# Kernel optimization log

Measured on AMD Instinct MI355X. Metric: run time of the kernel, lower is better.

The kernel has to match this reference:

```python
import jax, jax.numpy as jnp
import numpy as np

B, CIN, H, W = 8, 3, 128, 128
D_MODEL = 256
N_LAYERS = 4
D_STATE = 16
D_CONV = 4
EXPAND = 2
HEADDIM = 64
D_INNER = EXPAND * D_MODEL            # 512
NHEADS = D_INNER // HEADDIM           # 8
CONV_DIM = D_INNER + 2 * D_STATE      # 544
D_IN_PROJ = 2 * D_INNER + 2 * D_STATE + NHEADS  # 1064
D_OUT = 10
EPS = 1e-5


def setup_inputs() -> dict:
    key = jax.random.key(0)
    ks = iter(jax.random.split(key, 64))
    nrm = lambda shape, s=0.02: jax.random.normal(next(ks), shape, jnp.float32) * s
    L = N_LAYERS
    # dt init in [1e-3, 0.1], dt_bias = inverse softplus of dt
    dt = jnp.exp(jax.random.uniform(next(ks), (L, NHEADS)) * (np.log(0.1) - np.log(1e-3)) + np.log(1e-3))
    dt_bias = dt + jnp.log(-jnp.expm1(-dt))
    A_log = jnp.log(jax.random.uniform(next(ks), (L, NHEADS), minval=1.0, maxval=16.0))
    return {
        "x": jax.random.normal(next(ks), (B, CIN, H, W), jnp.float32),
        "stem_w1": nrm((D_MODEL // 2, CIN, 3, 3), 0.1),
        "stem_g1": jnp.ones((D_MODEL // 2,), jnp.float32),
        "stem_b1": jnp.zeros((D_MODEL // 2,), jnp.float32),
        "stem_w2": nrm((D_MODEL, D_MODEL // 2, 4, 4), 0.05),
        "stem_g2": jnp.ones((D_MODEL,), jnp.float32),
        "stem_b2": jnp.zeros((D_MODEL,), jnp.float32),
        "in_w": nrm((L, D_MODEL, D_IN_PROJ)),
        "conv_w": nrm((L, CONV_DIM, D_CONV), 0.2),
        "conv_b": jnp.zeros((L, CONV_DIM), jnp.float32),
        "dt_bias": dt_bias,
        "A_log": A_log,
        "D_skip": jnp.ones((L, NHEADS), jnp.float32),
        "rms_w": jnp.ones((L, D_INNER), jnp.float32),
        "out_w": nrm((L, D_INNER, D_MODEL)),
        "ln_g": jnp.ones((L, D_MODEL), jnp.float32),
        "ln_b": jnp.zeros((L, D_MODEL), jnp.float32),
        "head_ln_g": jnp.ones((D_MODEL,), jnp.float32),
        "head_ln_b": jnp.zeros((D_MODEL,), jnp.float32),
        "head_w": nrm((D_MODEL, D_OUT)),
        "head_b": jnp.zeros((D_OUT,), jnp.float32),
    }


def _bn(x, g, b):  # eval-mode BatchNorm2d with running mean 0 / var 1
    return x * g[None, :, None, None] + b[None, :, None, None]


def _ln(x, g, b):
    m = jnp.mean(x, -1, keepdims=True)
    v = jnp.mean((x - m) ** 2, -1, keepdims=True)
    return (x - m) * jax.lax.rsqrt(v + EPS) * g + b


def _mamba2(x, in_w, conv_w, conv_b, dt_bias, A_log, D_skip, rms_w, out_w):
    Bb, Lq, _ = x.shape
    zxbcdt = x @ in_w                                        # (B,L,D_IN_PROJ)
    z = zxbcdt[..., :D_INNER]
    xBC = zxbcdt[..., D_INNER:D_INNER + CONV_DIM]
    dt = jax.nn.softplus(zxbcdt[..., -NHEADS:] + dt_bias)    # (B,L,H)
    # causal depthwise conv1d over time
    xp = jnp.pad(xBC, ((0, 0), (D_CONV - 1, 0), (0, 0)))
    xBC = sum(xp[:, k:k + Lq, :] * conv_w[:, k] for k in range(D_CONV)) + conv_b
    xBC = jax.nn.silu(xBC)
    xs = xBC[..., :D_INNER].reshape(Bb, Lq, NHEADS, HEADDIM)       # (B,L,H,P)
    Bm = xBC[..., D_INNER:D_INNER + D_STATE]                        # (B,L,N)
    Cm = xBC[..., D_INNER + D_STATE:]                               # (B,L,N)
    dA = jnp.exp(dt * (-jnp.exp(A_log)))                            # (B,L,H)
    dtx = xs * dt[..., None]                                        # (B,L,H,P)

    def step(h, inp):  # h: (B,H,P,N)
        dA_t, dtx_t, B_t, C_t = inp
        h = h * dA_t[:, :, None, None] + dtx_t[..., None] * B_t[:, None, None, :]
        y = jnp.einsum('bhpn,bn->bhp', h, C_t)
        return h, y

    h0 = jnp.zeros((Bb, NHEADS, HEADDIM, D_STATE), x.dtype)
    seq = (jnp.moveaxis(dA, 1, 0), jnp.moveaxis(dtx, 1, 0),
           jnp.moveaxis(Bm, 1, 0), jnp.moveaxis(Cm, 1, 0))
    _, ys = jax.lax.scan(step, h0, seq)                             # (L,B,H,P)
    y = jnp.moveaxis(ys, 0, 1) + xs * D_skip[None, None, :, None]
    y = y.reshape(Bb, Lq, D_INNER)
    y = y * jax.nn.silu(z)                                          # gated
    y = y * jax.lax.rsqrt(jnp.mean(y * y, -1, keepdims=True) + EPS) * rms_w
    return y @ out_w


def reference(x, stem_w1, stem_g1, stem_b1, stem_w2, stem_g2, stem_b2,
              in_w, conv_w, conv_b, dt_bias, A_log, D_skip, rms_w, out_w,
              ln_g, ln_b, head_ln_g, head_ln_b, head_w, head_b):
    dn = ('NCHW', 'OIHW', 'NCHW')
    h = jax.lax.conv_general_dilated(x, stem_w1, (1, 1), 'SAME', dimension_numbers=dn)
    h = jax.nn.gelu(_bn(h, stem_g1, stem_b1), approximate=False)
    h = jax.lax.conv_general_dilated(h, stem_w2, (4, 4), 'VALID', dimension_numbers=dn)
    h = jax.nn.gelu(_bn(h, stem_g2, stem_b2), approximate=False)
    tok = h.reshape(h.shape[0], D_MODEL, -1).transpose(0, 2, 1)     # (B,L,D)
    for i in range(N_LAYERS):
        m = _mamba2(tok, in_w[i], conv_w[i], conv_b[i], dt_bias[i],
                    A_log[i], D_skip[i], rms_w[i], out_w[i])
        tok = _ln(m + tok, ln_g[i], ln_b[i])
    pooled = tok.mean(1)
    return _ln(pooled, head_ln_g, head_ln_b) @ head_w + head_b
```

## Files before the change

### kernel.cpp

```cpp
#include <hip/hip_runtime.h>
#include <hip/hip_bf16.h>


#define DEV __device__ __forceinline__
typedef __hip_bfloat16 bf16;
typedef unsigned short ushort_t;
typedef __attribute__((ext_vector_type(8))) short s8v;
typedef __attribute__((ext_vector_type(8))) unsigned short u8v;
typedef __attribute__((ext_vector_type(4))) unsigned short u4v;
typedef __attribute__((ext_vector_type(4))) float f4v;

#define CHUNK 32
#define NCH 32
#define YST 520

#define SP_CONVW 0
#define SP_CONVB 8704
#define SP_DTB   10880
#define SP_ALOG  10912
#define SP_DSK   10944
#define SP_RMSW  10976
#define SP_LNG   13024
#define SP_LNB   14048
#define SP_HLG   15072
#define SP_HLB   15328
#define SP_HW    15584
#define SP_HB    18144
#define SP_G1    18160
#define SP_B1    18288
#define SP_G2    18416
#define SP_B2    18672
#define SP_TOTAL 18928

DEV float bf2f(bf16 h) { return __bfloat162float(h); }
DEV bf16 f2bf(float f) { return __float2bfloat16(f); }
DEV float us2f(ushort_t u) { return __uint_as_float(((unsigned int)u) << 16); }
DEV ushort_t f2bfs(float f) {
    unsigned int u = __float_as_uint(f);
    return (ushort_t)((u + 0x7FFFu + ((u >> 16) & 1u)) >> 16);
}
DEV float ldf(const void* p, size_t i, int bf) {
    return bf ? us2f(((const ushort_t*)p)[i]) : ((const float*)p)[i];
}
DEV ushort_t ldbf(const void* p, size_t i, int bf) {
    return bf ? ((const ushort_t*)p)[i] : f2bfs(((const float*)p)[i]);
}
DEV int mode_of(const void* g1) { return (((const unsigned int*)g1)[0] == 0x3F800000u) ? 0 : 1; }
DEV float sigmoidf_(float x) { return 1.f / (1.f + __expf(-x)); }
DEV float geluf_(float x) { return 0.5f * x * (1.f + erff(x * 0.70710678118654752f)); }

__global__ void k_prep(const void* cw, const void* cb, const void* dtb, const void* alog,
                       const void* dsk, const void* rmsw, const void* lng, const void* lnb,
                       const void* hlg, const void* hlb, const void* hw, const void* hb,
                       const void* g1, const void* b1, const void* g2, const void* b2,
                       const void* w1, const void* w2, const void* inw, const void* outw,
                       float* __restrict__ sp, ushort_t* __restrict__ wT) {
    int md = mode_of(g1);
    int i = blockIdx.x * 256 + threadIdx.x;
    if (i < SP_TOTAL) {
        float v;
        if (i < SP_CONVB) v = ldf(cw, i, md);
        else if (i < SP_DTB) v = ldf(cb, i - SP_CONVB, md);
        else if (i < SP_ALOG) v = ldf(dtb, i - SP_DTB, md);
        else if (i < SP_DSK) v = ldf(alog, i - SP_ALOG, md);
        else if (i < SP_RMSW) v = ldf(dsk, i - SP_DSK, md);
        else if (i < SP_LNG) v = ldf(rmsw, i - SP_RMSW, md);
        else if (i < SP_LNB) v = ldf(lng, i - SP_LNG, md);
        else if (i < SP_HLG) v = ldf(lnb, i - SP_LNB, md);
        else if (i < SP_HLB) v = ldf(hlg, i - SP_HLG, md);
        else if (i < SP_HW) v = ldf(hlb, i - SP_HLB, md);
        else if (i < SP_HB) v = ldf(hw, i - SP_HW, md);
        else if (i < SP_G1) v = (i - SP_HB < 10) ? ldf(hb, i - SP_HB, md) : 0.f;
        else if (i < SP_B1) v = ldf(g1, i - SP_G1, md);
        else if (i < SP_G2) v = ldf(b1, i - SP_B1, md);
        else if (i < SP_B2) v = ldf(g2, i - SP_G2, md);
        else v = ldf(b2, i - SP_B2, md);
        sp[i] = v;
        return;
    }
    int iw = i - SP_TOTAL;
    if (iw >= 2142208) return;
    ushort_t v;
    if (iw < 4096) {
        int oc = iw >> 5, k = iw & 31;
        v = (k < 27) ? ldbf(w1, (size_t)oc * 27 + k, md) : 0;
    } else if (iw < 528384) {
        int j = iw - 4096;
        int oc = j >> 11, k = j & 2047;
        int c = k & 127, kykx = k >> 7;
        v = ldbf(w2, (size_t)(oc * 128 + c) * 16 + kykx, md);
    } else if (iw < 1617920) {
        int j = iw - 528384;
        int l = j / 272384, r = j % 272384;
        int n = r >> 8, k = r & 255;
        v = ldbf(inw, (size_t)l * 272384 + (size_t)k * 1064 + n, md);
    } else {
        int j = iw - 1617920;
        int l = j >> 17, r = j & 131071;
        int n = r >> 9, k = r & 511;
        v = ldbf(outw, (size_t)l * 131072 + (size_t)k * 256 + n, md);
    }
    wT[iw] = v;
}

template <int MD>
DEV void im2col_body(const void* x, ushort_t* __restrict__ Aim, int m) {
    int xx = m & 127;
    int y = (m >> 7) & 127;
    int b = m >> 14;
    ushort_t* o = Aim + (size_t)m * 32;
#pragma unroll
    for (int ci = 0; ci < 3; ci++)
#pragma unroll
        for (int dy = 0; dy < 3; dy++) {
            int sy = y + dy - 1;
#pragma unroll
            for (int dx = 0; dx < 3; dx++) {
                int sx = xx + dx - 1;
                ushort_t v = 0;
                if (sy >= 0 && sy < 128 && sx >= 0 && sx < 128) {
                    size_t idx = (size_t)((b * 3 + ci) * 128 + sy) * 128 + sx;
                    v = MD ? ((const ushort_t*)x)[idx] : f2bfs(((const float*)x)[idx]);
                }
                o[ci * 9 + dy * 3 + dx] = v;
            }
        }
#pragma unroll
    for (int k = 27; k < 32; k++) o[k] = 0;
}
__global__ void k_im2col(const void* __restrict__ x, ushort_t* __restrict__ Aim,
                         const void* __restrict__ g1) {
    int m = blockIdx.x * 256 + threadIdx.x;
    if (m >= 131072) return;
    if (mode_of(g1)) im2col_body<1>(x, Aim, m);
    else im2col_body<0>(x, Aim, m);
}

template <int EPI, int CBF, int BK>
__global__ __launch_bounds__(256, 3) void k_gemmT(const ushort_t* __restrict__ A,
                                                  const ushort_t* __restrict__ Wt, void* __restrict__ C,
                                                  int M, int N, int K, int klen,
                                                  const float* __restrict__ g, const float* __restrict__ bb) {
    constexpr int KG = BK / 8;
    constexpr int EA = BK / 4;
    constexpr int EB = BK / 2;
    constexpr int AU = EA / 8;
    constexpr int BU = EB / 8;
    __shared__ __align__(16) ushort_t As[2][64 * BK];
    __shared__ __align__(16) ushort_t Bs[2][128 * BK];
    int tid = threadIdx.x;
    int m0 = blockIdx.y * 64, n0 = blockIdx.x * 128;
    int koff = blockIdx.z * klen;
    int w = tid >> 6, lane = tid & 63;
    int wm = (w >> 1) * 32, wn = (w & 1) * 64;
    int lm = lane & 15, quad = lane >> 4;
    int ar = tid >> 2, ak = (tid & 3) * EA;
    int br = tid >> 1, bk = (tid & 1) * EB;
    bool bvalid = (n0 + br) < N;

    u8v pa[AU], pb[BU];
    auto loadT = [&](int kb) {
        const u8v* ap = (const u8v*)(A + (size_t)(m0 + ar) * K + koff + kb + ak);
#pragma unroll
        for (int j = 0; j < AU; j++) pa[j] = ap[j];
        if (bvalid) {
            const u8v* bp = (const u8v*)(Wt + (size_t)(n0 + br) * K + koff + kb + bk);
#pragma unroll
            for (int j = 0; j < BU; j++) pb[j] = bp[j];
        } else {
#pragma unroll
            for (int j = 0; j < BU; j++) pb[j] = (u8v)0;
        }
    };
    auto storeT = [&](int buf) {
        int ag = ak >> 3;
#pragma unroll
        for (int j = 0; j < AU; j++)
            *(u8v*)&As[buf][((ar >> 4) * KG + ag + j) * 128 + (ar & 15) * 8] = pa[j];
        int bg = bk >> 3;
#pragma unroll
        for (int j = 0; j < BU; j++)
            *(u8v*)&Bs[buf][((br >> 4) * KG + bg + j) * 128 + (br & 15) * 8] = pb[j];
    };

    f4v acc[2][4];
#pragma unroll
    for (int i = 0; i < 2; i++)
#pragma unroll
        for (int j = 0; j < 4; j++) acc[i][j] = (f4v){0.f, 0.f, 0.f, 0.f};

    int niter = klen / BK;
    loadT(0);
    storeT(0);
    if (niter > 1) loadT(BK);
    __syncthreads();
    for (int it = 0; it < niter; it++) {
        int buf = it & 1;
        if (it + 1 < niter) {
            storeT(buf ^ 1);
            if (it + 2 < niter) loadT((it + 2) * BK);
        }
#pragma unroll
        for (int kk = 0; kk < BK / 32; kk++) {
            s8v af[2], bfr[4];
#pragma unroll
            for (int i = 0; i < 2; i++)
                af[i] = *(const s8v*)&As[buf][(((wm >> 4) + i) * KG + kk * 4 + quad) * 128 + lm * 8];
#pragma unroll
            for (int j = 0; j < 4; j++)
                bfr[j] = *(const s8v*)&Bs[buf][(((wn >> 4) + j) * KG + kk * 4 + quad) * 128 + lm * 8];
#pragma unroll
            for (int i = 0; i < 2; i++)
#pragma unroll
                for (int j = 0; j < 4; j++)
                    acc[i][j] = __builtin_amdgcn_mfma_f32_16x16x32_bf16(af[i], bfr[j], acc[i][j], 0, 0, 0);
        }
        __syncthreads();
    }
    float* Cz = (float*)C + (size_t)blockIdx.z * M * N;
#pragma unroll
    for (int i = 0; i < 2; i++)
#pragma unroll
        for (int j = 0; j < 4; j++) {
            int nn = n0 + wn + j * 16 + lm;
            if (nn >= N) continue;
            float gv = (EPI >= 1) ? g[nn] : 0.f, bv = (EPI >= 1) ? bb[nn] : 0.f;
#pragma unroll
            for (int rr = 0; rr < 4; rr++) {
                int mm = m0 + wm + i * 16 + quad * 4 + rr;
                float v = acc[i][j][rr];
                if (EPI >= 1) v = geluf_(v * gv + bv);
                if (EPI == 2) {
                    int b = mm >> 14, y = (mm >> 7) & 127, x = mm & 127;
                    size_t mp = (size_t)(b * 1024 + (y >> 2) * 32 + (x >> 2));
                    ((bf16*)C)[mp * 2048 + ((y & 3) * 4 + (x & 3)) * 128 + nn] = f2bf(v);
                } else if (CBF) {
                    ((bf16*)C)[(size_t)mm * N + nn] = f2bf(v);
                } else {
                    Cz[(size_t)mm * N + nn] = v;
                }
            }
        }
}

__global__ __launch_bounds__(256) void k_stemred(const float* __restrict__ parts, const float* __restrict__ sp,
                                                 float* __restrict__ tok, ushort_t* __restrict__ tokb) {
    int m = blockIdx.x, c = threadIdx.x;
    size_t off = (size_t)m * 256 + c;
    float s = parts[off] + parts[2097152 + off];
    float v = geluf_(s * sp[SP_G2 + c] + sp[SP_B2 + c]);
    tok[off] = v;
    tokb[off] = f2bfs(v);
}

__global__ __launch_bounds__(64) void k_scan1(const bf16* __restrict__ zx, const float* __restrict__ sp,
                                              float* __restrict__ Sbuf, float* __restrict__ Pbuf, int layer) {
    int bid = blockIdx.x;
    int c = bid & (NCH - 1);
    int bh = bid >> 5;
    int b = bh >> 3, h = bh & 7;
    int p = threadIdx.x;
    __shared__ __align__(16) ushort_t zraw[35 * 64];
    __shared__ __align__(16) ushort_t braw[35 * 32];
    __shared__ float xs_s[CHUNK * 64];
    __shared__ __align__(16) float bc_s[CHUNK * 32];
    __shared__ float da_s[CHUNK], dt_s[CHUNK];
    const ushort_t* zxB = (const ushort_t*)zx + (size_t)b * 1024 * 1064;
    int t0 = c * CHUNK;
#pragma unroll
    for (int k = 0; k < 5; k++) {
        int j = p + k * 64;
        if (j < 280) {
            int row = j >> 3, c8 = j & 7;
            int t = t0 - 3 + row;
            u8v v = (u8v)0;
            if (t >= 0) v = *(const u8v*)(zxB + (size_t)t * 1064 + 512 + h * 64 + c8 * 8);
            *(u8v*)&zraw[row * 64 + c8 * 8] = v;
        }
    }
#pragma unroll
    for (int k = 0; k < 3; k++) {
        int j = p + k * 64;
        if (j < 140) {
            int row = j >> 2, c8 = j & 3;
            int t = t0 - 3 + row;
            u8v v = (u8v)0;
            if (t >= 0) v = *(const u8v*)(zxB + (size_t)t * 1064 + 1024 + c8 * 8);
            *(u8v*)&braw[row * 32 + c8 * 8] = v;
        }
    }
    if (p < CHUNK) {
        float raw = bf2f(zx[(size_t)(b * 1024 + t0 + p) * 1064 + 1056 + h]) + sp[SP_DTB + layer * 8 + h];
        float dt = raw > 20.f ? raw : log1pf(expf(raw));
        float a = expf(sp[SP_ALOG + layer * 8 + h]);
        dt_s[p] = dt;
        da_s[p] = expf(-dt * a);
    }
    __syncthreads();
    {
        const float* wp = sp + SP_CONVW + (size_t)(layer * 544 + h * 64 + p) * 4;
        float w0 = wp[0], w1 = wp[1], w2 = wp[2], w3 = wp[3];
        float bias = sp[SP_CONVB + layer * 544 + h * 64 + p];
#pragma unroll 8
        for (int tt = 0; tt < CHUNK; tt++) {
            float acc = bias + us2f(zraw[tt * 64 + p]) * w0 + us2f(zraw[(tt + 1) * 64 + p]) * w1 +
                        us2f(zraw[(tt + 2) * 64 + p]) * w2 + us2f(zraw[(tt + 3) * 64 + p]) * w3;
            xs_s[tt * 64 + p] = acc * sigmoidf_(acc);
        }
    }
    if (p < 32) {
        const float* wp = sp + SP_CONVW + (size_t)(layer * 544 + 512 + p) * 4;
        float w0 = wp[0], w1 = wp[1], w2 = wp[2], w3 = wp[3];
        float bias = sp[SP_CONVB + layer * 544 + 512 + p];
        int n = p & 15;
        int slot = (p < 16) ? 2 * n : 2 * n + 1;
#pragma unroll 8
        for (int tt = 0; tt < CHUNK; tt++) {
            float acc = bias + us2f(braw[tt * 32 + p]) * w0 + us2f(braw[(tt + 1) * 32 + p]) * w1 +
                        us2f(braw[(tt + 2) * 32 + p]) * w2 + us2f(braw[(tt + 3) * 32 + p]) * w3;
            bc_s[tt * 32 + slot] = acc * sigmoidf_(acc);
        }
    }
    __syncthreads();
    float hs[16];
#pragma unroll
    for (int n = 0; n < 16; n++) hs[n] = 0.f;
    float P = 1.f;
    for (int tt = 0; tt < CHUNK; tt++) {
        float xsv = xs_s[tt * 64 + p];
        float dAv = da_s[tt], dtv = dt_s[tt];
        P *= dAv;
        float dtx = xsv * dtv;
        const float4* bcp = (const float4*)&bc_s[tt * 32];
#pragma unroll
        for (int j = 0; j < 8; j++) {
            float4 v = bcp[j];
            hs[2 * j] = hs[2 * j] * dAv + dtx * v.x;
            hs[2 * j + 1] = hs[2 * j + 1] * dAv + dtx * v.z;
        }
    }
    float* So = Sbuf + (size_t)bid * 1024;
#pragma unroll
    for (int n = 0; n < 16; n++) So[n * 64 + p] = hs[n];
    if (p == 0) Pbuf[bid] = P;
}

__global__ __launch_bounds__(256) void k_scan2(const float* __restrict__ Sbuf, const float* __restrict__ Pbuf,
                                               float* __restrict__ Hbuf) {
    int bh = blockIdx.x >> 2;
    int e = ((blockIdx.x & 3) << 8) + threadIdx.x;
    const float* Sp = Sbuf + (size_t)bh * NCH * 1024 + e;
    float* Hp = Hbuf + (size_t)bh * NCH * 1024 + e;
    float hh = 0.f;
#pragma unroll
    for (int gq = 0; gq < 4; gq++) {
        float s[8];
#pragma unroll
        for (int c2 = 0; c2 < 8; c2++) s[c2] = Sp[(size_t)(gq * 8 + c2) * 1024];
#pragma unroll
        for (int c2 = 0; c2 < 8; c2++) {
            Hp[(size_t)(gq * 8 + c2) * 1024] = hh;
            float P = Pbuf[bh * NCH + gq * 8 + c2];
            hh = P * hh + s[c2];
        }
    }
}

__global__ __launch_bounds__(512, 2) void k_scan3go(const bf16* __restrict__ zx,
                                                    const float* __restrict__ Hbuf,
                                                    const float* __restrict__ sp,
                                                    const ushort_t* __restrict__ Wt,
                                                    float* __restrict__ tok, ushort_t* __restrict__ tokb,
                                                    int layer) {
    int bid = blockIdx.x;
    int c = bid & 31;
    int b = bid >> 5;
    int tid = threadIdx.x;
    int h = tid >> 6, p = tid & 63;
    __shared__ __align__(16) ushort_t zraw[35 * 512];
    __shared__ __align__(16) ushort_t braw[35 * 32];
    __shared__ __align__(16) float bc_s[CHUNK * 32];
    __shared__ float da_s[8 * CHUNK], dt_s[8 * CHUNK];
    const ushort_t* zxB = (const ushort_t*)zx + (size_t)b * 1024 * 1064;
    int t0 = c * CHUNK;

#pragma unroll
    for (int k = 0; k < 5; k++) {
        int j = tid + k * 512;
        if (j < 2240) {
            int row = j >> 6, c8 = j & 63;
            int t = t0 - 3 + row;
            u8v v = (u8v)0;
            if (t >= 0) v = *(const u8v*)(zxB + (size_t)t * 1064 + 512 + c8 * 8);
            *(u8v*)&zraw[row * 512 + c8 * 8] = v;
        }
    }
    if (tid < 140) {
        int row = tid >> 2, c8 = tid & 3;
        int t = t0 - 3 + row;
        u8v v = (u8v)0;
        if (t >= 0) v = *(const u8v*)(zxB + (size_t)t * 1064 + 1024 + c8 * 8);
        *(u8v*)&braw[row * 32 + c8 * 8] = v;
    }
    if (tid < 256) {
        int tt = tid >> 3, hh = tid & 7;
        float raw = bf2f(zx[(size_t)(b * 1024 + t0 + tt) * 1064 + 1056 + hh]) + sp[SP_DTB + layer * 8 + hh];
        float dtv = raw > 20.f ? raw : log1pf(expf(raw));
        float a = expf(sp[SP_ALOG + layer * 8 + hh]);
        dt_s[hh * 32 + tt] = dtv;
        da_s[hh * 32 + tt] = expf(-dtv * a);
    }
    __syncthreads();

    float xs[CHUNK];
    {
        float4 w4 = *(const float4*)(sp + SP_CONVW + (size_t)(layer * 544 + tid) * 4);
        float bias = sp[SP_CONVB + layer * 544 + tid];
#pragma unroll
        for (int tt = 0; tt < CHUNK; tt++) {
            float acc = bias + us2f(zraw[tt * 512 + tid]) * w4.x + us2f(zraw[(tt + 1) * 512 + tid]) * w4.y +
                        us2f(zraw[(tt + 2) * 512 + tid]) * w4.z + us2f(zraw[(tt + 3) * 512 + tid]) * w4.w;
            xs[tt] = acc * sigmoidf_(acc);
        }
    }
    if (tid < 32) {
        float4 w4 = *(const float4*)(sp + SP_CONVW + (size_t)(layer * 544 + 512 + tid) * 4);
        float bias = sp[SP_CONVB + layer * 544 + 512 + tid];
        int n = tid & 15;
        int slot = (tid < 16) ? 2 * n : 2 * n + 1;
#pragma unroll
        for (int tt = 0; tt < CHUNK; tt++) {
            float acc = bias + us2f(braw[tt * 32 + tid]) * w4.x + us2f(braw[(tt + 1) * 32 + tid]) * w4.y +
                        us2f(braw[(tt + 2) * 32 + tid]) * w4.z + us2f(braw[(tt + 3) * 32 + tid]) * w4.w;
            bc_s[tt * 32 + slot] = acc * sigmoidf_(acc);
        }
    }

    float hs[16];
    {
        const float* Si = Hbuf + ((size_t)(b * 8 + h) * 32 + c) * 1024;
#pragma unroll
        for (int n = 0; n < 16; n++) hs[n] = Si[n * 64 + p];
    }
    float dsk = sp[SP_DSK + layer * 8 + h];
    __syncthreads();

    ushort_t* y_s = zraw;
#pragma unroll
    for (int tt = 0; tt < CHUNK; tt++) {
        float dAv = da_s[h * 32 + tt], dtv = dt_s[h * 32 + tt];
        float dtx = xs[tt] * dtv;
        float acc = 0.f;
        const float4* bcp = (const float4*)&bc_s[tt * 32];
#pragma unroll
        for (int j = 0; j < 8; j++) {
            float4 v = bcp[j];
            hs[2 * j] = hs[2 * j] * dAv + dtx * v.x;
            acc += hs[2 * j] * v.y;
            hs[2 * j + 1] = hs[2 * j + 1] * dAv + dtx * v.z;
            acc += hs[2 * j + 1] * v.w;
        }
        y_s[tt * YST + tid] = f2bfs(acc + xs[tt] * dsk);
    }
    __syncthreads();

    {
        int lane = p;
        float4 rw0 = *(const float4*)(sp + SP_RMSW + layer * 512 + lane * 8);
        float4 rw1 = *(const float4*)(sp + SP_RMSW + layer * 512 + lane * 8 + 4);
        float rwv[8] = {rw0.x, rw0.y, rw0.z, rw0.w, rw1.x, rw1.y, rw1.z, rw1.w};
#pragma unroll
        for (int r = 0; r < 4; r++) {
            int tt = h * 4 + r;
            u8v yv = *(const u8v*)&y_s[tt * YST + lane * 8];
            u8v zv = *(const u8v*)(zxB + (size_t)(t0 + tt) * 1064 + lane * 8);
            float t[8];
            float ss = 0.f;
#pragma unroll
            for (int j2 = 0; j2 < 8; j2++) {
                float z = us2f(zv[j2]);
                float yy = us2f(yv[j2]);
                float tv = yy * (z * sigmoidf_(z));
                t[j2] = tv;
                ss += tv * tv;
            }
#pragma unroll
            for (int d = 32; d; d >>= 1) ss += __shfl_xor(ss, d, 64);
            float scale = rsqrtf(ss * (1.f / 512.f) + 1e-5f);
            u8v o;
#pragma unroll
            for (int j2 = 0; j2 < 8; j2++) o[j2] = f2bfs(t[j2] * scale * rwv[j2]);
            *(u8v*)&y_s[tt * YST + lane * 8] = o;
        }
    }
    __syncthreads();

    int lm = p & 15, quad = p >> 4;
    f4v acc2[2][2];
#pragma unroll
    for (int mi = 0; mi < 2; mi++)
#pragma unroll
        for (int ni = 0; ni < 2; ni++) acc2[mi][ni] = (f4v){0.f, 0.f, 0.f, 0.f};
#pragma unroll
    for (int kk = 0; kk < 16; kk++) {
        s8v af[2], bw[2];
#pragma unroll
        for (int mi = 0; mi < 2; mi++)
            af[mi] = *(const s8v*)&y_s[(mi * 16 + lm) * YST + kk * 32 + quad * 8];
#pragma unroll
        for (int ni = 0; ni < 2; ni++)
            bw[ni] = *(const s8v*)(Wt + (size_t)(h * 32 + ni * 16 + lm) * 512 + kk * 32 + quad * 8);
#pragma unroll
        for (int mi = 0; mi < 2; mi++)
#pragma unroll
            for (int ni = 0; ni < 2; ni++)
                acc2[mi][ni] = __builtin_amdgcn_mfma_f32_16x16x32_bf16(af[mi], bw[ni], acc2[mi][ni], 0, 0, 0);
    }
    __syncthreads();

    float* C_lds = (float*)zraw;
#pragma unroll
    for (int mi = 0; mi < 2; mi++)
#pragma unroll
        for (int ni = 0; ni < 2; ni++)
#pragma unroll
            for (int rr = 0; rr < 4; rr++)
                C_lds[(mi * 16 + quad * 4 + rr) * 260 + h * 32 + ni * 16 + lm] = acc2[mi][ni][rr];
    __syncthreads();

#pragma unroll
    for (int r = 0; r < 4; r++) {
        int tt = h * 4 + r;
        size_t off = (size_t)(b * 1024 + t0 + tt) * 256 + p * 4;
        float4 v = *(const float4*)(tok + off);
        float4 cv = *(const float4*)&C_lds[tt * 260 + p * 4];
        v.x += cv.x;
        v.y += cv.y;
        v.z += cv.z;
        v.w += cv.w;
        float s = v.x + v.y + v.z + v.w;
#pragma unroll
        for (int d = 32; d; d >>= 1) s += __shfl_xor(s, d, 64);
        float mean = s * (1.f / 256.f);
        float dx = v.x - mean, dy = v.y - mean, dz = v.z - mean, dw = v.w - mean;
        float ss = dx * dx + dy * dy + dz * dz + dw * dw;
#pragma unroll
        for (int d = 32; d; d >>= 1) ss += __shfl_xor(ss, d, 64);
        float inv = rsqrtf(ss * (1.f / 256.f) + 1e-5f);
        const float* lg = sp + SP_LNG + layer * 256 + p * 4;
        const float* lb = sp + SP_LNB + layer * 256 + p * 4;
        float r0 = dx * inv * lg[0] + lb[0];
        float r1 = dy * inv * lg[1] + lb[1];
        float r2 = dz * inv * lg[2] + lb[2];
        float r3 = dw * inv * lg[3] + lb[3];
        float4 rv;
        rv.x = r0; rv.y = r1; rv.z = r2; rv.w = r3;
        *(float4*)(tok + off) = rv;
        u4v ob;
        ob[0] = f2bfs(r0); ob[1] = f2bfs(r1); ob[2] = f2bfs(r2); ob[3] = f2bfs(r3);
        *(u4v*)(tokb + off) = ob;
    }
}

DEV float block_sum256(float v, float* s4) {
#pragma unroll
    for (int off = 32; off; off >>= 1) v += __shfl_down(v, off, 64);
    __syncthreads();
    if ((threadIdx.x & 63) == 0) s4[threadIdx.x >> 6] = v;
    __syncthreads();
    return s4[0] + s4[1] + s4[2] + s4[3];
}

__global__ void k_pool1(const float* __restrict__ tok, float* __restrict__ ppart) {
    int b = blockIdx.x >> 4, chunk = blockIdx.x & 15;
    int c = threadIdx.x;
    float s = 0.f;
    for (int t = 0; t < 64; t++) s += tok[((size_t)b * 1024 + chunk * 64 + t) * 256 + c];
    ppart[(size_t)blockIdx.x * 256 + c] = s;
}

__global__ __launch_bounds__(256) void k_head(const float* __restrict__ ppart, const float* __restrict__ sp,
                                              void* __restrict__ out, const void* __restrict__ g1) {
    __shared__ float s4[4];
    __shared__ float lds[256];
    int md = mode_of(g1);
    int b = blockIdx.x;
    int c = threadIdx.x;
    float v = 0.f;
#pragma unroll
    for (int k = 0; k < 16; k++) v += ppart[(size_t)(b * 16 + k) * 256 + c];
    v *= (1.f / 1024.f);
    float mean = block_sum256(v, s4) * (1.f / 256.f);
    float d = v - mean;
    float var = block_sum256(d * d, s4) * (1.f / 256.f);
    lds[c] = d * rsqrtf(var + 1e-5f) * sp[SP_HLG + c] + sp[SP_HLB + c];
    __syncthreads();
    if (c < 10) {
        float s = sp[SP_HB + c];
        for (int k = 0; k < 256; k++) s += lds[k] * sp[SP_HW + k * 10 + c];
        if (md)
            ((bf16*)out)[b * 10 + c] = f2bf(s);
        else
            ((float*)out)[b * 10 + c] = s;
    }
}

extern "C" void kernel_launch(void* const* d_in, const int* in_sizes, int n_in, void* d_out, int out_size,
                              void* d_ws, size_t ws_size, hipStream_t stream) {
    const void* x         = d_in[0];
    const void* stem_w1   = d_in[1];
    const void* stem_g1   = d_in[2];
    const void* stem_b1   = d_in[3];
    const void* stem_w2   = d_in[4];
    const void* stem_g2   = d_in[5];
    const void* stem_b2   = d_in[6];
    const void* in_w      = d_in[7];
    const void* conv_w    = d_in[8];
    const void* conv_b    = d_in[9];
    const void* dt_bias   = d_in[10];
    const void* A_log     = d_in[11];
    const void* D_skip    = d_in[12];
    const void* rms_w     = d_in[13];
    const void* out_w     = d_in[14];
    const void* ln_g      = d_in[15];
    const void* ln_b      = d_in[16];
    const void* head_ln_g = d_in[17];
    const void* head_ln_b = d_in[18];
    const void* head_w    = d_in[19];
    const void* head_b    = d_in[20];

    float* ws     = (float*)d_ws;
    float* tok    = ws;
    float* mbuf   = ws + 2097152;
    float* Hbuf   = ws + 4194304;
    float* parts  = ws + 6291456;
    float* ppart  = ws + 14682112;
    float* Pbuf   = ws + 14714880;
    float* sp     = ws + 14716944;
    ushort_t* tokb = (ushort_t*)(ws + 14735888);
    ushort_t* wT  = (ushort_t*)(ws + 15784464);
    ushort_t* w1T   = wT;
    ushort_t* w2T   = wT + 4096;
    ushort_t* inwT  = wT + 528384;
    ushort_t* outwT = wT + 1617920;
    bf16* arena   = (bf16*)(ws + 16855568);
    bf16* zx      = arena;
    ushort_t* patch = (ushort_t*)arena;
    ushort_t* Aim  = (ushort_t*)mbuf;
    float* Sbuf    = mbuf;

    k_prep<<<(SP_TOTAL + 2142208 + 255) / 256, 256, 0, stream>>>(
        conv_w, conv_b, dt_bias, A_log, D_skip, rms_w, ln_g, ln_b, head_ln_g, head_ln_b, head_w, head_b,
        stem_g1, stem_b1, stem_g2, stem_b2, stem_w1, stem_w2, in_w, out_w, sp, wT);

    k_im2col<<<512, 256, 0, stream>>>(x, Aim, stem_g1);
    k_gemmT<2, 1, 32><<<dim3(1, 2048, 1), 256, 0, stream>>>(Aim, w1T, patch, 131072, 128, 32, 32,
                                                            sp + SP_G1, sp + SP_B1);
    k_gemmT<0, 0, 64><<<dim3(2, 128, 2), 256, 0, stream>>>(patch, w2T, parts, 8192, 256, 2048, 1024,
                                                           nullptr, nullptr);
    k_stemred<<<8192, 256, 0, stream>>>(parts, sp, tok, tokb);

    for (int l = 0; l < 4; l++) {
        k_gemmT<0, 1, 64><<<dim3(9, 128, 1), 256, 0, stream>>>(tokb, inwT + (size_t)l * 272384, zx, 8192,
                                                               1064, 256, 256, nullptr, nullptr);
        k_scan1<<<2048, 64, 0, stream>>>(zx, sp, Sbuf, Pbuf, l);
        k_scan2<<<256, 256, 0, stream>>>(Sbuf, Pbuf, Hbuf);
        k_scan3go<<<256, 512, 0, stream>>>(zx, Hbuf, sp, outwT + (size_t)l * 131072, tok, tokb, l);
    }

    k_pool1<<<128, 256, 0, stream>>>(tok, ppart);
    k_head<<<8, 256, 0, stream>>>(ppart, sp, d_out, stem_g1);
}
```

Measured before the change: 461.8 us.

## Fuse im2col into stem GEMM, vectorize stemred, merge heads in scan1 blocks

Removes the separate im2col kernel by computing the 3x3 patch gather directly inside the first stem GEMM's A-tile load, which avoids writing and re-reading a 131072x32 bf16 buffer. k_stemred now processes four channels per thread with float4 loads and stores. k_scan1 switches to one 512-thread block per (batch, chunk) that covers all 8 heads, so the shared B/C convolution and dt values are computed once instead of once per head, and x values stay in registers. In exchange the fused gather issues scattered scalar global loads inside the GEMM, and the scan has far fewer blocks (256) with higher register use.

```diff
diff --git a/kernel.cpp b/kernel.cpp
--- a/kernel.cpp
+++ b/kernel.cpp
@@ -103,44 +103,13 @@
     wT[iw] = v;
 }
 
-template <int MD>
-DEV void im2col_body(const void* x, ushort_t* __restrict__ Aim, int m) {
-    int xx = m & 127;
-    int y = (m >> 7) & 127;
-    int b = m >> 14;
-    ushort_t* o = Aim + (size_t)m * 32;
-#pragma unroll
-    for (int ci = 0; ci < 3; ci++)
-#pragma unroll
-        for (int dy = 0; dy < 3; dy++) {
-            int sy = y + dy - 1;
-#pragma unroll
-            for (int dx = 0; dx < 3; dx++) {
-                int sx = xx + dx - 1;
-                ushort_t v = 0;
-                if (sy >= 0 && sy < 128 && sx >= 0 && sx < 128) {
-                    size_t idx = (size_t)((b * 3 + ci) * 128 + sy) * 128 + sx;
-                    v = MD ? ((const ushort_t*)x)[idx] : f2bfs(((const float*)x)[idx]);
-                }
-                o[ci * 9 + dy * 3 + dx] = v;
-            }
-        }
-#pragma unroll
-    for (int k = 27; k < 32; k++) o[k] = 0;
-}
-__global__ void k_im2col(const void* __restrict__ x, ushort_t* __restrict__ Aim,
-                         const void* __restrict__ g1) {
-    int m = blockIdx.x * 256 + threadIdx.x;
-    if (m >= 131072) return;
-    if (mode_of(g1)) im2col_body<1>(x, Aim, m);
-    else im2col_body<0>(x, Aim, m);
-}
-
-template <int EPI, int CBF, int BK>
+template <int EPI, int CBF, int BK, int IMC>
 __global__ __launch_bounds__(256, 3) void k_gemmT(const ushort_t* __restrict__ A,
                                                   const ushort_t* __restrict__ Wt, void* __restrict__ C,
                                                   int M, int N, int K, int klen,
-                                                  const float* __restrict__ g, const float* __restrict__ bb) {
+                                                  const float* __restrict__ g, const float* __restrict__ bb,
+                                                  const void* __restrict__ xsrc,
+                                                  const void* __restrict__ g1p) {
     constexpr int KG = BK / 8;
     constexpr int EA = BK / 4;
     constexpr int EB = BK / 2;
@@ -157,12 +126,34 @@
     int ar = tid >> 2, ak = (tid & 3) * EA;
     int br = tid >> 1, bk = (tid & 1) * EB;
     bool bvalid = (n0 + br) < N;
+    int md = 0;
+    if constexpr (IMC) md = mode_of(g1p);
 
     u8v pa[AU], pb[BU];
     auto loadT = [&](int kb) {
-        const u8v* ap = (const u8v*)(A + (size_t)(m0 + ar) * K + koff + kb + ak);
-#pragma unroll
-        for (int j = 0; j < AU; j++) pa[j] = ap[j];
+        if constexpr (IMC) {
+            int m = m0 + ar;
+            int xx2 = m & 127, yy2 = (m >> 7) & 127, bb2 = m >> 14;
+            u8v v = (u8v)0;
+#pragma unroll
+            for (int j = 0; j < 8; j++) {
+                int k = ak + j;
+                if (k < 27) {
+                    int ci = k / 9, r2 = k - ci * 9;
+                    int dy = r2 / 3, dx = r2 - dy * 3;
+                    int sy = yy2 + dy - 1, sx = xx2 + dx - 1;
+                    if (sy >= 0 && sy < 128 && sx >= 0 && sx < 128) {
+                        size_t idx = ((size_t)(bb2 * 3 + ci) * 128 + sy) * 128 + sx;
+                        v[j] = md ? ((const ushort_t*)xsrc)[idx] : f2bfs(((const float*)xsrc)[idx]);
+                    }
+                }
+            }
+            pa[0] = v;
+        } else {
+            const u8v* ap = (const u8v*)(A + (size_t)(m0 + ar) * K + koff + kb + ak);
+#pragma unroll
+            for (int j = 0; j < AU; j++) pa[j] = ap[j];
+        }
         if (bvalid) {
             const u8v* bp = (const u8v*)(Wt + (size_t)(n0 + br) * K + koff + kb + bk);
 #pragma unroll
@@ -245,92 +236,101 @@
 
 __global__ __launch_bounds__(256) void k_stemred(const float* __restrict__ parts, const float* __restrict__ sp,
                                                  float* __restrict__ tok, ushort_t* __restrict__ tokb) {
-    int m = blockIdx.x, c = threadIdx.x;
-    size_t off = (size_t)m * 256 + c;
-    float s = parts[off] + parts[2097152 + off];
-    float v = geluf_(s * sp[SP_G2 + c] + sp[SP_B2 + c]);
-    tok[off] = v;
-    tokb[off] = f2bfs(v);
-}
-
-__global__ __launch_bounds__(64) void k_scan1(const bf16* __restrict__ zx, const float* __restrict__ sp,
-                                              float* __restrict__ Sbuf, float* __restrict__ Pbuf, int layer) {
+    size_t off = ((size_t)blockIdx.x * 256 + threadIdx.x) * 4;
+    float4 p0 = *(const float4*)(parts + off);
+    float4 p1 = *(const float4*)(parts + 2097152 + off);
+    int c = (int)(off & 255);
+    const float* gg = sp + SP_G2 + c;
+    const float* bp = sp + SP_B2 + c;
+    float v0 = geluf_((p0.x + p1.x) * gg[0] + bp[0]);
+    float v1 = geluf_((p0.y + p1.y) * gg[1] + bp[1]);
+    float v2 = geluf_((p0.z + p1.z) * gg[2] + bp[2]);
+    float v3 = geluf_((p0.w + p1.w) * gg[3] + bp[3]);
+    float4 o;
+    o.x = v0; o.y = v1; o.z = v2; o.w = v3;
+    *(float4*)(tok + off) = o;
+    u4v ob;
+    ob[0] = f2bfs(v0); ob[1] = f2bfs(v1); ob[2] = f2bfs(v2); ob[3] = f2bfs(v3);
+    *(u4v*)(tokb + off) = ob;
+}
+
+__global__ __launch_bounds__(512, 2) void k_scan1(const bf16* __restrict__ zx, const float* __restrict__ sp,
+                                                  float* __restrict__ Sbuf, float* __restrict__ Pbuf,
+                                                  int layer) {
     int bid = blockIdx.x;
-    int c = bid & (NCH - 1);
-    int bh = bid >> 5;
-    int b = bh >> 3, h = bh & 7;
-    int p = threadIdx.x;
-    __shared__ __align__(16) ushort_t zraw[35 * 64];
+    int c = bid & 31;
+    int b = bid >> 5;
+    int tid = threadIdx.x;
+    int h = tid >> 6, p = tid & 63;
+    __shared__ __align__(16) ushort_t zraw[35 * 512];
     __shared__ __align__(16) ushort_t braw[35 * 32];
-    __shared__ float xs_s[CHUNK * 64];
     __shared__ __align__(16) float bc_s[CHUNK * 32];
-    __shared__ float da_s[CHUNK], dt_s[CHUNK];
+    __shared__ float da_s[8 * CHUNK], dt_s[8 * CHUNK];
     const ushort_t* zxB = (const ushort_t*)zx + (size_t)b * 1024 * 1064;
     int t0 = c * CHUNK;
+
 #pragma unroll
     for (int k = 0; k < 5; k++) {
-        int j = p + k * 64;
-        if (j < 280) {
-            int row = j >> 3, c8 = j & 7;
+        int j = tid + k * 512;
+        if (j < 2240) {
+            int row = j >> 6, c8 = j & 63;
             int t = t0 - 3 + row;
             u8v v = (u8v)0;
-            if (t >= 0) v = *(const u8v*)(zxB + (size_t)t * 1064 + 512 + h * 64 + c8 * 8);
-            *(u8v*)&zraw[row * 64 + c8 * 8] = v;
-        }
-    }
-#pragma unroll
-    for (int k = 0; k < 3; k++) {
-        int j = p + k * 64;
-        if (j < 140) {
-            int row = j >> 2, c8 = j & 3;
-            int t = t0 - 3 + row;
-            u8v v = (u8v)0;
-            if (t >= 0) v = *(const u8v*)(zxB + (size_t)t * 1064 + 1024 + c8 * 8);
-            *(u8v*)&braw[row * 32 + c8 * 8] = v;
-        }
-    }
-    if (p < CHUNK) {
-        float raw = bf2f(zx[(size_t)(b * 1024 + t0 + p) * 1064 + 1056 + h]) + sp[SP_DTB + layer * 8 + h];
-        float dt = raw > 20.f ? raw : log1pf(expf(raw));
-        float a = expf(sp[SP_ALOG + layer * 8 + h]);
-        dt_s[p] = dt;
-        da_s[p] = expf(-dt * a);
-    }
-    __syncthreads();
+            if (t >= 0) v = *(const u8v*)(zxB + (size_t)t * 1064 + 512 + c8 * 8);
+            *(u8v*)&zraw[row * 512 + c8 * 8] = v;
+        }
+    }
+    if (tid < 140) {
+        int row = tid >> 2, c8 = tid & 3;
+        int t = t0 - 3 + row;
+        u8v v = (u8v)0;
+        if (t >= 0) v = *(const u8v*)(zxB + (size_t)t * 1064 + 1024 + c8 * 8);
+        *(u8v*)&braw[row * 32 + c8 * 8] = v;
+    }
+    if (tid < 256) {
+        int tt = tid >> 3, hh = tid & 7;
+        float raw = bf2f(zx[(size_t)(b * 1024 + t0 + tt) * 1064 + 1056 + hh]) + sp[SP_DTB + layer * 8 + hh];
+        float dtv = raw > 20.f ? raw : log1pf(expf(raw));
+        float a = expf(sp[SP_ALOG + layer * 8 + hh]);
+        dt_s[hh * 32 + tt] = dtv;
+        da_s[hh * 32 + tt] = expf(-dtv * a);
+    }
+    __syncthreads();
+
+    float xs[CHUNK];
     {
-        const float* wp = sp + SP_CONVW + (size_t)(layer * 544 + h * 64 + p) * 4;
-        float w0 = wp[0], w1 = wp[1], w2 = wp[2], w3 = wp[3];
-        float bias = sp[SP_CONVB + layer * 544 + h * 64 + p];
-#pragma unroll 8
+        float4 w4 = *(const float4*)(sp + SP_CONVW + (size_t)(layer * 544 + tid) * 4);
+        float bias = sp[SP_CONVB + layer * 544 + tid];
+#pragma unroll
         for (int tt = 0; tt < CHUNK; tt++) {
-            float acc = bias + us2f(zraw[tt * 64 + p]) * w0 + us2f(zraw[(tt + 1) * 64 + p]) * w1 +
-                        us2f(zraw[(tt + 2) * 64 + p]) * w2 + us2f(zraw[(tt + 3) * 64 + p]) * w3;
-            xs_s[tt * 64 + p] = acc * sigmoidf_(acc);
-        }
-    }
-    if (p < 32) {
-        const float* wp = sp + SP_CONVW + (size_t)(layer * 544 + 512 + p) * 4;
-        float w0 = wp[0], w1 = wp[1], w2 = wp[2], w3 = wp[3];
-        float bias = sp[SP_CONVB + layer * 544 + 512 + p];
-        int n = p & 15;
-        int slot = (p < 16) ? 2 * n : 2 * n + 1;
-#pragma unroll 8
+            float acc = bias + us2f(zraw[tt * 512 + tid]) * w4.x + us2f(zraw[(tt + 1) * 512 + tid]) * w4.y +
+                        us2f(zraw[(tt + 2) * 512 + tid]) * w4.z + us2f(zraw[(tt + 3) * 512 + tid]) * w4.w;
+            xs[tt] = acc * sigmoidf_(acc);
+        }
+    }
+    if (tid < 32) {
+        float4 w4 = *(const float4*)(sp + SP_CONVW + (size_t)(layer * 544 + 512 + tid) * 4);
+        float bias = sp[SP_CONVB + layer * 544 + 512 + tid];
+        int n = tid & 15;
+        int slot = (tid < 16) ? 2 * n : 2 * n + 1;
+#pragma unroll
         for (int tt = 0; tt < CHUNK; tt++) {
-            float acc = bias + us2f(braw[tt * 32 + p]) * w0 + us2f(braw[(tt + 1) * 32 + p]) * w1 +
-                        us2f(braw[(tt + 2) * 32 + p]) * w2 + us2f(braw[(tt + 3) * 32 + p]) * w3;
+            float acc = bias + us2f(braw[tt * 32 + tid]) * w4.x + us2f(braw[(tt + 1) * 32 + tid]) * w4.y +
+                        us2f(braw[(tt + 2) * 32 + tid]) * w4.z + us2f(braw[(tt + 3) * 32 + tid]) * w4.w;
             bc_s[tt * 32 + slot] = acc * sigmoidf_(acc);
         }
     }
     __syncthreads();
+
     float hs[16];
 #pragma unroll
     for (int n = 0; n < 16; n++) hs[n] = 0.f;
     float P = 1.f;
+#pragma unroll
     for (int tt = 0; tt < CHUNK; tt++) {
-        float xsv = xs_s[tt * 64 + p];
-        float dAv = da_s[tt], dtv = dt_s[tt];
+        float dAv = da_s[h * 32 + tt], dtv = dt_s[h * 32 + tt];
         P *= dAv;
-        float dtx = xsv * dtv;
+        float dtx = xs[tt] * dtv;
         const float4* bcp = (const float4*)&bc_s[tt * 32];
 #pragma unroll
         for (int j = 0; j < 8; j++) {
@@ -339,10 +339,10 @@
             hs[2 * j + 1] = hs[2 * j + 1] * dAv + dtx * v.z;
         }
     }
-    float* So = Sbuf + (size_t)bid * 1024;
+    float* So = Sbuf + ((size_t)(b * 8 + h) * 32 + c) * 1024;
 #pragma unroll
     for (int n = 0; n < 16; n++) So[n * 64 + p] = hs[n];
-    if (p == 0) Pbuf[bid] = P;
+    if (p == 0) Pbuf[(b * 8 + h) * 32 + c] = P;
 }
 
 __global__ __launch_bounds__(256) void k_scan2(const float* __restrict__ Sbuf, const float* __restrict__ Pbuf,
@@ -646,24 +646,22 @@
     bf16* arena   = (bf16*)(ws + 16855568);
     bf16* zx      = arena;
     ushort_t* patch = (ushort_t*)arena;
-    ushort_t* Aim  = (ushort_t*)mbuf;
     float* Sbuf    = mbuf;
 
     k_prep<<<(SP_TOTAL + 2142208 + 255) / 256, 256, 0, stream>>>(
         conv_w, conv_b, dt_bias, A_log, D_skip, rms_w, ln_g, ln_b, head_ln_g, head_ln_b, head_w, head_b,
         stem_g1, stem_b1, stem_g2, stem_b2, stem_w1, stem_w2, in_w, out_w, sp, wT);
 
-    k_im2col<<<512, 256, 0, stream>>>(x, Aim, stem_g1);
-    k_gemmT<2, 1, 32><<<dim3(1, 2048, 1), 256, 0, stream>>>(Aim, w1T, patch, 131072, 128, 32, 32,
-                                                            sp + SP_G1, sp + SP_B1);
-    k_gemmT<0, 0, 64><<<dim3(2, 128, 2), 256, 0, stream>>>(patch, w2T, parts, 8192, 256, 2048, 1024,
-                                                           nullptr, nullptr);
-    k_stemred<<<8192, 256, 0, stream>>>(parts, sp, tok, tokb);
+    k_gemmT<2, 1, 32, 1><<<dim3(1, 2048, 1), 256, 0, stream>>>(
+        (const ushort_t*)x, w1T, patch, 131072, 128, 32, 32, sp + SP_G1, sp + SP_B1, x, stem_g1);
+    k_gemmT<0, 0, 64, 0><<<dim3(2, 128, 2), 256, 0, stream>>>(
+        patch, w2T, parts, 8192, 256, 2048, 1024, nullptr, nullptr, nullptr, nullptr);
+    k_stemred<<<2048, 256, 0, stream>>>(parts, sp, tok, tokb);
 
     for (int l = 0; l < 4; l++) {
-        k_gemmT<0, 1, 64><<<dim3(9, 128, 1), 256, 0, stream>>>(tokb, inwT + (size_t)l * 272384, zx, 8192,
-                                                               1064, 256, 256, nullptr, nullptr);
-        k_scan1<<<2048, 64, 0, stream>>>(zx, sp, Sbuf, Pbuf, l);
+        k_gemmT<0, 1, 64, 0><<<dim3(9, 128, 1), 256, 0, stream>>>(
+            tokb, inwT + (size_t)l * 272384, zx, 8192, 1064, 256, 256, nullptr, nullptr, nullptr, nullptr);
+        k_scan1<<<256, 512, 0, stream>>>(zx, sp, Sbuf, Pbuf, l);
         k_scan2<<<256, 256, 0, stream>>>(Sbuf, Pbuf, Hbuf);
         k_scan3go<<<256, 512, 0, stream>>>(zx, Hbuf, sp, outwT + (size_t)l * 131072, tok, tokb, l);
     }
```

After: 439.6 us (median of 2 runs). -4.8%, faster.
